# Optimization experiments

Hardware: AMD Instinct MI355X
Metric: run time of the kernel (lower is better)

Reference implementation:

```python
import jax, jax.numpy as jnp
import numpy as np

TAU_MEM = 20.0
TAU_SYN = 5.0
ALPHA_MEM = float(np.exp(-1.0 / TAU_MEM))
ALPHA_SYN = float(np.exp(-1.0 / TAU_SYN))
CONNECTIVITY = 0.1
SPECTRAL_RADIUS = 0.9


def setup_inputs() -> dict:
    key = jax.random.key(0)
    k1, k2, k3, k4 = jax.random.split(key, 4)
    B, D, N = 2048, 256, 512
    rates = jax.random.normal(k1, (B, D), dtype=jnp.float32)
    input_weight = jax.random.normal(k2, (N, D), dtype=jnp.float32) * 0.1
    W = jax.random.normal(k3, (N, N), dtype=jnp.float32)
    mask = (jax.random.uniform(k4, (N, N)) < CONNECTIVITY).astype(jnp.float32)
    W = W * mask
    # mirror torch init: scale by spectral_radius / max eigvalsh
    max_eig = jnp.linalg.eigvalsh(W)[-1]
    W = W * (SPECTRAL_RADIUS / max_eig)
    return {
        "rates": rates,
        "input_weight": input_weight,
        "reservoir_weight": W,
        "v_mem": jnp.zeros((B, N), dtype=jnp.float32),
        "current": jnp.zeros((B, N), dtype=jnp.float32),
        "n_steps": 64,
    }


def reference(rates, input_weight, reservoir_weight, v_mem, current, n_steps):
    dtype = rates.dtype
    # input current is identical every step in the original loop -> hoist it
    input_current = rates @ input_weight.T  # (B, N)

    def step(carry, _):
        v, c, spike_sum = carry
        rec = (c > 0).astype(dtype) @ reservoir_weight  # (B, N)
        c = ALPHA_SYN * c + (1.0 - ALPHA_SYN) * (input_current + rec)
        v = ALPHA_MEM * v + (1.0 - ALPHA_MEM) * c
        spike_sum = spike_sum + (v > 0).astype(dtype)
        return (v, c, spike_sum), None

    (v, c, spike_sum), _ = jax.lax.scan(
        step, (v_mem, current, jnp.zeros_like(v_mem)), None, length=n_steps
    )
    readout = spike_sum / n_steps  # == stack(spikes).mean(dim=1)
    return readout, (v, c)
```

## Files before the change

kernel.cpp:

```cpp
#include <hip/hip_runtime.h>
#include <stdint.h>


#define N_NEU 512
#define B_ROWS 2048
#define D_IN 256
#define R_PB 8
#define NBLK (B_ROWS / R_PB)

#define WS_PERM    0
#define WS_RANK    2048
#define WS_CNT     4096
#define WS_CNTW    8192
#define WS_IBASE   8256
#define WS_WBASE   8320
#define WS_IDX     16384
#define WS_WT      81920

#define SPK_OFF(k)  ((k) << 4)
#define SPK_BUF     8192

#define H16_ONE 0x3C00u

__global__ __launch_bounds__(256) void lsm_count(
    const float* __restrict__ W, uint32_t* __restrict__ ws)
{
    int t  = threadIdx.x;
    int k0 = blockIdx.x * 4;
    int c0 = 0, c1 = 0;
    #pragma unroll
    for (int kk = 0; kk < 4; ++kk) {
        const float* row = W + (size_t)(k0 + kk) * N_NEU;
        c0 += (row[t]       != 0.0f) ? 1 : 0;
        c1 += (row[t + 256] != 0.0f) ? 1 : 0;
    }
    if (c0) atomicAdd(&ws[(WS_CNT >> 2) + t],       (uint32_t)c0);
    if (c1) atomicAdd(&ws[(WS_CNT >> 2) + t + 256], (uint32_t)c1);
}

__global__ __launch_bounds__(512) void lsm_sort(uint32_t* __restrict__ ws)
{
    __shared__ int hist[N_NEU + 1];
    __shared__ int csort[N_NEU];
    __shared__ int gcw[8];

    int t = threadIdx.x;
    int creal = (int)ws[(WS_CNT >> 2) + t];
    for (int i = t; i < N_NEU + 1; i += 512) hist[i] = 0;
    __syncthreads();
    atomicAdd(&hist[creal], 1);
    __syncthreads();
    if (t == 0) {
        int acc = 0;
        for (int v = 0; v <= N_NEU; ++v) { int h = hist[v]; hist[v] = acc; acc += h; }
    }
    __syncthreads();
    int rank = atomicAdd(&hist[creal], 1);
    ws[(WS_PERM >> 2) + rank] = (uint32_t)t;
    ws[(WS_RANK >> 2) + t]    = (uint32_t)rank;
    csort[rank] = creal;
    __syncthreads();
    if (t < 8) {
        int cw = csort[t * 64 + 63];
        cw = (cw + 7) & ~7;
        gcw[t] = cw;
        ws[(WS_CNTW >> 2) + t] = (uint32_t)cw;
    }
    __syncthreads();
    if (t == 0) {
        int ai = 0, aw = 0;
        for (int g = 0; g < 8; ++g) {
            ws[(WS_IBASE >> 2) + g] = (uint32_t)ai;
            ws[(WS_WBASE >> 2) + g] = (uint32_t)aw;
            ai += gcw[g] * 64 * 2;
            aw += gcw[g] * 64 * 4;
        }
    }
    __syncthreads();
    int wg = rank >> 6, ls = rank & 63;
    int cw = gcw[wg];
    uint32_t ib = ws[(WS_IBASE >> 2) + wg];
    uint32_t wb = ws[(WS_WBASE >> 2) + wg];
    char* base = (char*)ws;
    for (int j = creal; j < cw; ++j) {
        *(unsigned short*)(base + WS_IDX + ib + (j >> 3) * 1024 + ls * 16 + (j & 7) * 2) = 0;
        *(float*)(base + WS_WT + wb + (j >> 3) * 2048 + ls * 32 + (j & 7) * 4) = 0.0f;
    }
}

__global__ __launch_bounds__(64) void lsm_fill(
    const float* __restrict__ W, uint32_t* __restrict__ ws)
{
    int c    = blockIdx.x;
    int lane = threadIdx.x;
    char* base = (char*)ws;
    uint32_t rank = ws[(WS_RANK >> 2) + c];
    int wg = (int)(rank >> 6), ls = (int)(rank & 63);
    uint32_t ib = ws[(WS_IBASE >> 2) + wg];
    uint32_t wb = ws[(WS_WBASE >> 2) + wg];
    int rot = ls & 7;

    __shared__ int bcnt[8];
    __shared__ int bcur[8];
    if (lane < 8) bcnt[lane] = 0;
    __syncthreads();

    for (int k = lane; k < N_NEU; k += 64) {
        float wv = W[(size_t)k * N_NEU + c];
        if (wv != 0.0f) {
            int r = ((k & 7) - rot) & 7;
            atomicAdd(&bcnt[r], 1);
        }
    }
    __syncthreads();
    if (lane == 0) {
        int acc = 0;
        for (int r = 0; r < 8; ++r) { bcur[r] = acc; acc += bcnt[r]; }
    }
    __syncthreads();

    for (int k = lane; k < N_NEU; k += 64) {
        float wv = W[(size_t)k * N_NEU + c];
        if (wv != 0.0f) {
            int r = ((k & 7) - rot) & 7;
            int j = atomicAdd(&bcur[r], 1);
            *(unsigned short*)(base + WS_IDX + ib + (j >> 3) * 1024 + ls * 16 + (j & 7) * 2)
                = (unsigned short)SPK_OFF(k);
            *(float*)(base + WS_WT + wb + (j >> 3) * 2048 + ls * 32 + (j & 7) * 4) = wv;
        }
    }
}

#define GATH(P, X, B) \
    P##0 = *(const uint4*)((B) + ((X).x & 0xffffu)); \
    P##1 = *(const uint4*)((B) + ((X).x >> 16));     \
    P##2 = *(const uint4*)((B) + ((X).y & 0xffffu)); \
    P##3 = *(const uint4*)((B) + ((X).y >> 16));     \
    P##4 = *(const uint4*)((B) + ((X).z & 0xffffu)); \
    P##5 = *(const uint4*)((B) + ((X).z >> 16));     \
    P##6 = *(const uint4*)((B) + ((X).w & 0xffffu)); \
    P##7 = *(const uint4*)((B) + ((X).w >> 16));

#define FMIX_LO(ACC, WV, S) \
    asm("v_fma_mix_f32 %0, %1, %2, %0 op_sel:[0,0,0] op_sel_hi:[0,1,0]" \
        : "+v"(ACC) : "v"(WV), "v"(S));
#define FMIX_HI(ACC, WV, S) \
    asm("v_fma_mix_f32 %0, %1, %2, %0 op_sel:[0,1,0] op_sel_hi:[0,1,0]" \
        : "+v"(ACC) : "v"(WV), "v"(S));

#define C1(S, WV) \
    FMIX_LO(rec0, WV, (S).x) FMIX_HI(rec1, WV, (S).x) \
    FMIX_LO(rec2, WV, (S).y) FMIX_HI(rec3, WV, (S).y) \
    FMIX_LO(rec4, WV, (S).z) FMIX_HI(rec5, WV, (S).z) \
    FMIX_LO(rec6, WV, (S).w) FMIX_HI(rec7, WV, (S).w)

#define CONS(P, WA, WB) \
    C1(P##0, (WA).x) C1(P##1, (WA).y) C1(P##2, (WA).z) C1(P##3, (WA).w) \
    C1(P##4, (WB).x) C1(P##5, (WB).y) C1(P##6, (WB).z) C1(P##7, (WB).w)

#define LDW(WA, WB, K) \
    WA = ((const float4*)(wp0 + (K) * 2048))[0]; \
    WB = ((const float4*)(wp0 + (K) * 2048))[1];

__global__ __launch_bounds__(512, 1)
void lsm_main(
    const float* __restrict__ rates, const float* __restrict__ inW,
    const float* __restrict__ vin,   const float* __restrict__ cin,
    const int* __restrict__ nsteps_p,
    const uint32_t* __restrict__ ws, float* __restrict__ out)
{
    __shared__ __align__(16) unsigned char smem[2 * SPK_BUF + 16384];
    float* stg = (float*)(smem + 2 * SPK_BUF);
    float* rl  = stg;

    int q    = threadIdx.x;
    int blk  = blockIdx.x;
    int r0   = blk * R_PB;
    int w    = q >> 6;
    int lane = q & 63;
    int wg   = (w < 4) ? w : (11 - w);
    int n    = (int)ws[(WS_PERM >> 2) + wg * 64 + lane];
    int cw   = (int)ws[(WS_CNTW >> 2) + wg];
    int nit  = cw >> 3;
    const char* ip0 = (const char*)ws + WS_IDX + ws[(WS_IBASE >> 2) + wg]
                    + lane * 16;
    const char* wp0 = (const char*)ws + WS_WT  + ws[(WS_WBASE >> 2) + wg]
                    + lane * 32;
    int spk_n = SPK_OFF(n);

    float c0v[R_PB], v0v[R_PB];
    #pragma unroll
    for (int r = 0; r < R_PB; ++r)
        stg[r * N_NEU + q] = cin[(size_t)(r0 + r) * N_NEU + q];
    __syncthreads();
    #pragma unroll
    for (int r = 0; r < R_PB; ++r) c0v[r] = stg[r * N_NEU + n];
    __syncthreads();
    #pragma unroll
    for (int r = 0; r < R_PB; ++r)
        stg[r * N_NEU + q] = vin[(size_t)(r0 + r) * N_NEU + q];
    __syncthreads();
    #pragma unroll
    for (int r = 0; r < R_PB; ++r) v0v[r] = stg[r * N_NEU + n];
    __syncthreads();

    ((float4*)rl)[q] = ((const float4*)(rates + (size_t)r0 * D_IN))[q];
    __syncthreads();

    float I[R_PB] = {0.f, 0.f, 0.f, 0.f, 0.f, 0.f, 0.f, 0.f};
    {
        const float4* wrow = (const float4*)(inW + (size_t)n * D_IN);
        for (int d4 = 0; d4 < D_IN / 4; ++d4) {
            float4 wv = wrow[d4];
            #pragma unroll
            for (int r = 0; r < R_PB; ++r) {
                const float* rr = rl + r * D_IN + d4 * 4;
                I[r] += wv.x * rr[0] + wv.y * rr[1] + wv.z * rr[2] + wv.w * rr[3];
            }
        }
    }

    uint4 sini = make_uint4(0u, 0u, 0u, 0u);
    #pragma unroll
    for (int r = 0; r < R_PB; ++r) {
        unsigned hb = (c0v[r] > 0.f) ? H16_ONE : 0u;
        unsigned sh = (r & 1) ? 16 : 0;
        if (r < 2)      sini.x |= hb << sh;
        else if (r < 4) sini.y |= hb << sh;
        else if (r < 6) sini.z |= hb << sh;
        else            sini.w |= hb << sh;
    }
    *(uint4*)(smem + spk_n) = sini;

    unsigned ssx = 0u, ssy = 0u;

    uint4 xr0, xr1, xr2, xr3, xr4, xr5, xr6, xr7, xr8, xr9, xr10, xr11;
    const uint4 xz = make_uint4(0u, 0u, 0u, 0u);
    xr0  =              *(const uint4*)(ip0);
    xr1  = (1  < nit) ? *(const uint4*)(ip0 + 1024)  : xz;
    xr2  = (2  < nit) ? *(const uint4*)(ip0 + 2048)  : xz;
    xr3  = (3  < nit) ? *(const uint4*)(ip0 + 3072)  : xz;
    xr4  = (4  < nit) ? *(const uint4*)(ip0 + 4096)  : xz;
    xr5  = (5  < nit) ? *(const uint4*)(ip0 + 5120)  : xz;
    xr6  = (6  < nit) ? *(const uint4*)(ip0 + 6144)  : xz;
    xr7  = (7  < nit) ? *(const uint4*)(ip0 + 7168)  : xz;
    xr8  = (8  < nit) ? *(const uint4*)(ip0 + 8192)  : xz;
    xr9  = (9  < nit) ? *(const uint4*)(ip0 + 9216)  : xz;
    xr10 = (10 < nit) ? *(const uint4*)(ip0 + 10240) : xz;
    xr11 = (11 < nit) ? *(const uint4*)(ip0 + 11264) : xz;

    const float AS   = (float)0.8187307530779818;
    const float OMAS = (float)(1.0 - 0.8187307530779818);
    const float AM   = (float)0.9512294245007140;
    const float OMAM = (float)(1.0 - 0.9512294245007140);

    int T = nsteps_p[0];
    __syncthreads();

    #pragma unroll 1
    for (int t = 0; t < T; ++t) {
        const unsigned char* sb = smem + ((t & 1) ? SPK_BUF : 0);
        unsigned char*       db = smem + ((t & 1) ? 0 : SPK_BUF);

        float rec0 = 0.f, rec1 = 0.f, rec2 = 0.f, rec3 = 0.f;
        float rec4 = 0.f, rec5 = 0.f, rec6 = 0.f, rec7 = 0.f;
        uint4 a0, a1, a2, a3, a4, a5, a6, a7;
        uint4 b0, b1, b2, b3, b4, b5, b6, b7;
        float4 waA, wbA, waB, wbB;

        LDW(waA, wbA, 0)
        GATH(a, xr0, sb)
        if (1 < nit)  { LDW(waB, wbB, 1)  GATH(b, xr1, sb)  }
        CONS(a, waA, wbA)
        if (1 < nit)  {
            if (2 < nit)  { LDW(waA, wbA, 2)  GATH(a, xr2, sb)  }
            CONS(b, waB, wbB)
        }
        if (2 < nit)  {
            if (3 < nit)  { LDW(waB, wbB, 3)  GATH(b, xr3, sb)  }
            CONS(a, waA, wbA)
        }
        if (3 < nit)  {
            if (4 < nit)  { LDW(waA, wbA, 4)  GATH(a, xr4, sb)  }
            CONS(b, waB, wbB)
        }
        if (4 < nit)  {
            if (5 < nit)  { LDW(waB, wbB, 5)  GATH(b, xr5, sb)  }
            CONS(a, waA, wbA)
        }
        if (5 < nit)  {
            if (6 < nit)  { LDW(waA, wbA, 6)  GATH(a, xr6, sb)  }
            CONS(b, waB, wbB)
        }
        if (6 < nit)  {
            if (7 < nit)  { LDW(waB, wbB, 7)  GATH(b, xr7, sb)  }
            CONS(a, waA, wbA)
        }
        if (7 < nit)  {
            if (8 < nit)  { LDW(waA, wbA, 8)  GATH(a, xr8, sb)  }
            CONS(b, waB, wbB)
        }
        if (8 < nit)  {
            if (9 < nit)  { LDW(waB, wbB, 9)  GATH(b, xr9, sb)  }
            CONS(a, waA, wbA)
        }
        if (9 < nit)  {
            if (10 < nit) { LDW(waA, wbA, 10) GATH(a, xr10, sb) }
            CONS(b, waB, wbB)
        }
        if (10 < nit) {
            if (11 < nit) { LDW(waB, wbB, 11) GATH(b, xr11, sb) }
            CONS(a, waA, wbA)
        }
        if (11 < nit) {
            CONS(b, waB, wbB)
        }

        uint4 ns = make_uint4(0u, 0u, 0u, 0u);
        unsigned vbx = 0u, vby = 0u;
        {
            float rca[R_PB] = {rec0, rec1, rec2, rec3, rec4, rec5, rec6, rec7};
            #pragma unroll
            for (int r = 0; r < R_PB; ++r) {
                c0v[r] = AS * c0v[r] + OMAS * (I[r] + rca[r]);
                v0v[r] = AM * v0v[r] + OMAM * c0v[r];
                unsigned hb = (c0v[r] > 0.f) ? H16_ONE : 0u;
                unsigned vb = (v0v[r] > 0.f) ? 1u : 0u;
                unsigned sh = (r & 1) ? 16 : 0;
                if (r < 2)      ns.x |= hb << sh;
                else if (r < 4) ns.y |= hb << sh;
                else if (r < 6) ns.z |= hb << sh;
                else            ns.w |= hb << sh;
                if (r < 4) vbx |= vb << (r * 8);
                else       vby |= vb << ((r - 4) * 8);
            }
        }
        ssx += vbx;
        ssy += vby;
        *(uint4*)(db + spk_n) = ns;
        __syncthreads();
    }

    float invT = 1.0f / (float)T;
    size_t BN = (size_t)B_ROWS * N_NEU;

    #pragma unroll
    for (int r = 0; r < R_PB; ++r) {
        unsigned cnt = (r < 4) ? ((ssx >> (r * 8)) & 0xffu)
                               : ((ssy >> ((r - 4) * 8)) & 0xffu);
        stg[r * N_NEU + n] = (float)cnt * invT;
    }
    __syncthreads();
    #pragma unroll
    for (int r = 0; r < R_PB; ++r)
        out[(size_t)(r0 + r) * N_NEU + q] = stg[r * N_NEU + q];
    __syncthreads();

    #pragma unroll
    for (int r = 0; r < R_PB; ++r) stg[r * N_NEU + n] = v0v[r];
    __syncthreads();
    #pragma unroll
    for (int r = 0; r < R_PB; ++r)
        out[BN + (size_t)(r0 + r) * N_NEU + q] = stg[r * N_NEU + q];
    __syncthreads();

    #pragma unroll
    for (int r = 0; r < R_PB; ++r) stg[r * N_NEU + n] = c0v[r];
    __syncthreads();
    #pragma unroll
    for (int r = 0; r < R_PB; ++r)
        out[2 * BN + (size_t)(r0 + r) * N_NEU + q] = stg[r * N_NEU + q];
}

extern "C" void kernel_launch(void* const* d_in, const int* in_sizes, int n_in,
                              void* d_out, int out_size, void* d_ws, size_t ws_size,
                              hipStream_t stream)
{
    const float* rates = (const float*)d_in[0];
    const float* inW   = (const float*)d_in[1];
    const float* W     = (const float*)d_in[2];
    const float* vin   = (const float*)d_in[3];
    const float* cin   = (const float*)d_in[4];
    const int*   nst   = (const int*)d_in[5];
    uint32_t* ws = (uint32_t*)d_ws;
    float* out = (float*)d_out;
    (void)in_sizes; (void)n_in; (void)out_size; (void)ws_size;

    hipMemsetAsync((char*)d_ws + WS_CNT, 0, 2048, stream);

    lsm_count<<<128, 256, 0, stream>>>(W, ws);
    lsm_sort<<<1, 512, 0, stream>>>(ws);
    lsm_fill<<<N_NEU, 64, 0, stream>>>(W, ws);
    lsm_main<<<NBLK, 512, 0, stream>>>(rates, inW, vin, cin, nst, ws, out);
}
```

Measured before the change: 326.1 us.

## Schedule sparse index slots to spread LDS bank access across lanes per step

```diff
diff --git a/kernel.cpp b/kernel.cpp
--- a/kernel.cpp
+++ b/kernel.cpp
@@ -21,6 +21,8 @@
 #define SPK_BUF     8192
 
 #define H16_ONE 0x3C00u
+#define MAXPC   32
+#define MAXCW   96
 
 __global__ __launch_bounds__(256) void lsm_count(
     const float* __restrict__ W, uint32_t* __restrict__ ws)
@@ -76,58 +78,97 @@
             aw += gcw[g] * 64 * 4;
         }
     }
-    __syncthreads();
-    int wg = rank >> 6, ls = rank & 63;
-    int cw = gcw[wg];
-    uint32_t ib = ws[(WS_IBASE >> 2) + wg];
-    uint32_t wb = ws[(WS_WBASE >> 2) + wg];
-    char* base = (char*)ws;
-    for (int j = creal; j < cw; ++j) {
-        *(unsigned short*)(base + WS_IDX + ib + (j >> 3) * 1024 + ls * 16 + (j & 7) * 2) = 0;
-        *(float*)(base + WS_WT + wb + (j >> 3) * 2048 + ls * 32 + (j & 7) * 4) = 0.0f;
-    }
 }
 
 __global__ __launch_bounds__(64) void lsm_fill(
     const float* __restrict__ W, uint32_t* __restrict__ ws)
 {
-    int c    = blockIdx.x;
-    int lane = threadIdx.x;
+    int wg = blockIdx.x;
+    int ls = threadIdx.x;
     char* base = (char*)ws;
-    uint32_t rank = ws[(WS_RANK >> 2) + c];
-    int wg = (int)(rank >> 6), ls = (int)(rank & 63);
+
+    int c  = (int)ws[(WS_PERM >> 2) + wg * 64 + ls];
+    int cw = (int)ws[(WS_CNTW >> 2) + wg];
     uint32_t ib = ws[(WS_IBASE >> 2) + wg];
     uint32_t wb = ws[(WS_WBASE >> 2) + wg];
-    int rot = ls & 7;
-
-    __shared__ int bcnt[8];
-    __shared__ int bcur[8];
-    if (lane < 8) bcnt[lane] = 0;
-    __syncthreads();
-
-    for (int k = lane; k < N_NEU; k += 64) {
-        float wv = W[(size_t)k * N_NEU + c];
-        if (wv != 0.0f) {
-            int r = ((k & 7) - rot) & 7;
-            atomicAdd(&bcnt[r], 1);
-        }
-    }
-    __syncthreads();
-    if (lane == 0) {
-        int acc = 0;
-        for (int r = 0; r < 8; ++r) { bcur[r] = acc; acc += bcnt[r]; }
-    }
-    __syncthreads();
-
-    for (int k = lane; k < N_NEU; k += 64) {
-        float wv = W[(size_t)k * N_NEU + c];
-        if (wv != 0.0f) {
-            int r = ((k & 7) - rot) & 7;
-            int j = atomicAdd(&bcur[r], 1);
-            *(unsigned short*)(base + WS_IDX + ib + (j >> 3) * 1024 + ls * 16 + (j & 7) * 2)
-                = (unsigned short)SPK_OFF(k);
-            *(float*)(base + WS_WT + wb + (j >> 3) * 2048 + ls * 32 + (j & 7) * 4) = wv;
-        }
+
+    __shared__ unsigned short ent[64][8][MAXPC];
+    __shared__ unsigned short sched[64][98];
+    __shared__ int cap[8];
+
+    unsigned cl = 0, ch = 0;
+    int tot = 0;
+    for (int k0 = 0; k0 < N_NEU; k0 += 8) {
+        #pragma unroll
+        for (int rr = 0; rr < 8; ++rr) {
+            float wv = W[(size_t)(k0 + rr) * N_NEU + c];
+            if (wv != 0.0f) {
+                unsigned cnt = ((rr < 4) ? (cl >> (rr * 8))
+                                         : (ch >> ((rr - 4) * 8))) & 0xffu;
+                ent[ls][rr][cnt] = (unsigned short)(k0 + rr);
+                if (rr < 4) cl += 1u << (rr * 8);
+                else        ch += 1u << ((rr - 4) * 8);
+                ++tot;
+            }
+        }
+    }
+
+    for (int j = 0; j < cw; ++j) {
+        if (ls < 8) cap[ls] = 0;
+        __syncthreads();
+        int sel = -1;
+        if (tot > 0) {
+            int slack = (cw - j) - tot;
+            unsigned tried = 0;
+            for (int pass = 0; pass < 8 && sel < 0; ++pass) {
+                int best = -1; unsigned bv = 0;
+                #pragma unroll
+                for (int r = 0; r < 8; ++r) {
+                    unsigned v = ((r < 4) ? (cl >> (r * 8))
+                                          : (ch >> ((r - 4) * 8))) & 0xffu;
+                    if (!((tried >> r) & 1u) && v > bv) { bv = v; best = r; }
+                }
+                if (best < 0) break;
+                int old = atomicAdd(&cap[best], 1);
+                if (old < 8) sel = best;
+                else { atomicSub(&cap[best], 1); tried |= (1u << best); }
+            }
+            if (sel < 0 && slack <= 0) {
+                int best = 0; unsigned bv = 0;
+                #pragma unroll
+                for (int r = 0; r < 8; ++r) {
+                    unsigned v = ((r < 4) ? (cl >> (r * 8))
+                                          : (ch >> ((r - 4) * 8))) & 0xffu;
+                    if (v > bv) { bv = v; best = r; }
+                }
+                sel = best;
+            }
+        }
+        unsigned short sv = 0xffffu;
+        if (sel >= 0) {
+            unsigned v = ((sel < 4) ? (cl >> (sel * 8))
+                                    : (ch >> ((sel - 4) * 8))) & 0xffu;
+            sv = ent[ls][sel][(int)v - 1];
+            if (sel < 4) cl -= 1u << (sel * 8);
+            else         ch -= 1u << ((sel - 4) * 8);
+            --tot;
+        }
+        sched[ls][j] = sv;
+        __syncthreads();
+    }
+
+    for (int j = 0; j < cw; ++j) {
+        unsigned short sv = sched[ls][j];
+        unsigned short idxv; float wv;
+        if (sv != 0xffffu) {
+            idxv = (unsigned short)(sv << 4);
+            wv   = W[(size_t)sv * N_NEU + c];
+        } else {
+            idxv = (unsigned short)((j & 7) << 4);
+            wv   = 0.0f;
+        }
+        *(unsigned short*)(base + WS_IDX + ib + (j >> 3) * 1024 + ls * 16 + (j & 7) * 2) = idxv;
+        *(float*)(base + WS_WT + wb + (j >> 3) * 2048 + ls * 32 + (j & 7) * 4) = wv;
     }
 }
 
@@ -171,7 +212,6 @@
 {
     __shared__ __align__(16) unsigned char smem[2 * SPK_BUF + 16384];
     float* stg = (float*)(smem + 2 * SPK_BUF);
-    float* rl  = stg;
 
     int q    = threadIdx.x;
     int blk  = blockIdx.x;
@@ -204,18 +244,16 @@
     for (int r = 0; r < R_PB; ++r) v0v[r] = stg[r * N_NEU + n];
     __syncthreads();
 
-    ((float4*)rl)[q] = ((const float4*)(rates + (size_t)r0 * D_IN))[q];
-    __syncthreads();
-
     float I[R_PB] = {0.f, 0.f, 0.f, 0.f, 0.f, 0.f, 0.f, 0.f};
     {
         const float4* wrow = (const float4*)(inW + (size_t)n * D_IN);
+        const float4* rrow = (const float4*)(rates + (size_t)r0 * D_IN);
         for (int d4 = 0; d4 < D_IN / 4; ++d4) {
             float4 wv = wrow[d4];
             #pragma unroll
             for (int r = 0; r < R_PB; ++r) {
-                const float* rr = rl + r * D_IN + d4 * 4;
-                I[r] += wv.x * rr[0] + wv.y * rr[1] + wv.z * rr[2] + wv.w * rr[3];
+                float4 rv = rrow[r * (D_IN / 4) + d4];
+                I[r] += wv.x * rv.x + wv.y * rv.y + wv.z * rv.z + wv.w * rv.w;
             }
         }
     }
@@ -390,6 +428,6 @@
 
     lsm_count<<<128, 256, 0, stream>>>(W, ws);
     lsm_sort<<<1, 512, 0, stream>>>(ws);
-    lsm_fill<<<N_NEU, 64, 0, stream>>>(W, ws);
+    lsm_fill<<<8, 64, 0, stream>>>(W, ws);
     lsm_main<<<NBLK, 512, 0, stream>>>(rates, inW, vin, cin, nst, ws, out);
 }
```

Result: slower. 617.0 us (+89.2%).

## Rebuild sparse fill with row-residue buckets to balance LDS banks in gather

Applied to the files above, without the earlier changes.

```diff
diff --git a/kernel.cpp b/kernel.cpp
--- a/kernel.cpp
+++ b/kernel.cpp
@@ -21,6 +21,7 @@
 #define SPK_BUF     8192
 
 #define H16_ONE 0x3C00u
+#define MAXPC   24
 
 __global__ __launch_bounds__(256) void lsm_count(
     const float* __restrict__ W, uint32_t* __restrict__ ws)
@@ -76,57 +77,85 @@
             aw += gcw[g] * 64 * 4;
         }
     }
-    __syncthreads();
-    int wg = rank >> 6, ls = rank & 63;
-    int cw = gcw[wg];
-    uint32_t ib = ws[(WS_IBASE >> 2) + wg];
-    uint32_t wb = ws[(WS_WBASE >> 2) + wg];
-    char* base = (char*)ws;
-    for (int j = creal; j < cw; ++j) {
-        *(unsigned short*)(base + WS_IDX + ib + (j >> 3) * 1024 + ls * 16 + (j & 7) * 2) = 0;
-        *(float*)(base + WS_WT + wb + (j >> 3) * 2048 + ls * 32 + (j & 7) * 4) = 0.0f;
-    }
 }
 
-__global__ __launch_bounds__(64) void lsm_fill(
+__global__ __launch_bounds__(512) void lsm_fill(
     const float* __restrict__ W, uint32_t* __restrict__ ws)
 {
-    int c    = blockIdx.x;
-    int lane = threadIdx.x;
+    int g = blockIdx.x;
+    int t = threadIdx.x;
     char* base = (char*)ws;
-    uint32_t rank = ws[(WS_RANK >> 2) + c];
-    int wg = (int)(rank >> 6), ls = (int)(rank & 63);
-    uint32_t ib = ws[(WS_IBASE >> 2) + wg];
-    uint32_t wb = ws[(WS_WBASE >> 2) + wg];
-    int rot = ls & 7;
-
-    __shared__ int bcnt[8];
-    __shared__ int bcur[8];
-    if (lane < 8) bcnt[lane] = 0;
-    __syncthreads();
-
-    for (int k = lane; k < N_NEU; k += 64) {
-        float wv = W[(size_t)k * N_NEU + c];
-        if (wv != 0.0f) {
-            int r = ((k & 7) - rot) & 7;
-            atomicAdd(&bcnt[r], 1);
-        }
-    }
-    __syncthreads();
-    if (lane == 0) {
-        int acc = 0;
-        for (int r = 0; r < 8; ++r) { bcur[r] = acc; acc += bcnt[r]; }
-    }
-    __syncthreads();
-
-    for (int k = lane; k < N_NEU; k += 64) {
-        float wv = W[(size_t)k * N_NEU + c];
-        if (wv != 0.0f) {
-            int r = ((k & 7) - rot) & 7;
-            int j = atomicAdd(&bcur[r], 1);
-            *(unsigned short*)(base + WS_IDX + ib + (j >> 3) * 1024 + ls * 16 + (j & 7) * 2)
-                = (unsigned short)SPK_OFF(k);
-            *(float*)(base + WS_WT + wb + (j >> 3) * 2048 + ls * 32 + (j & 7) * 4) = wv;
+
+    __shared__ unsigned short ent_k[64][8][MAXPC];
+    __shared__ float          ent_w[64][8][MAXPC];
+
+    int rank = (int)ws[(WS_RANK >> 2) + t];
+    int ls   = rank & 63;
+    bool mine = ((rank >> 6) == g);
+
+    unsigned cl = 0, ch = 0;
+    for (int k0 = 0; k0 < N_NEU; k0 += 8) {
+        float wv[8];
+        #pragma unroll
+        for (int rr = 0; rr < 8; ++rr)
+            wv[rr] = W[(size_t)(k0 + rr) * N_NEU + t];
+        #pragma unroll
+        for (int rr = 0; rr < 8; ++rr) {
+            if (mine && wv[rr] != 0.0f) {
+                unsigned cnt = ((rr < 4) ? (cl >> (rr * 8))
+                                         : (ch >> ((rr - 4) * 8))) & 0xffu;
+                ent_k[ls][rr][cnt] = (unsigned short)(k0 + rr);
+                ent_w[ls][rr][cnt] = wv[rr];
+                if (rr < 4) cl += 1u << (rr * 8);
+                else        ch += 1u << ((rr - 4) * 8);
+            }
+        }
+    }
+
+    if (mine) {
+        int cw = (int)ws[(WS_CNTW >> 2) + g];
+        uint32_t ib = ws[(WS_IBASE >> 2) + g];
+        uint32_t wb = ws[(WS_WBASE >> 2) + g];
+        int Q = cw >> 3;
+
+        unsigned ul = 0, uh = 0;
+        int ovr = 0, ovi = Q;
+        while (ovr < 8) {
+            int nr = (int)(((ovr < 4) ? (cl >> (ovr * 8))
+                                      : (ch >> ((ovr - 4) * 8))) & 0xffu);
+            if (ovi < nr) break;
+            ++ovr; ovi = Q;
+        }
+
+        for (int j = 0; j < cw; ++j) {
+            int c = (j + ls) & 7;
+            int nc = (int)(((c < 4) ? (cl >> (c * 8))
+                                    : (ch >> ((c - 4) * 8))) & 0xffu);
+            int uc = (int)(((c < 4) ? (ul >> (c * 8))
+                                    : (uh >> ((c - 4) * 8))) & 0xffu);
+            int dc = (nc < Q) ? nc : Q;
+            unsigned short idxv; float wvv;
+            if (uc < dc) {
+                idxv = (unsigned short)SPK_OFF(ent_k[ls][c][uc]);
+                wvv  = ent_w[ls][c][uc];
+                if (c < 4) ul += 1u << (c * 8);
+                else       uh += 1u << ((c - 4) * 8);
+            } else if (ovr < 8) {
+                idxv = (unsigned short)SPK_OFF(ent_k[ls][ovr][ovi]);
+                wvv  = ent_w[ls][ovr][ovi];
+                ++ovi;
+                while (ovr < 8) {
+                    int nr = (int)(((ovr < 4) ? (cl >> (ovr * 8))
+                                              : (ch >> ((ovr - 4) * 8))) & 0xffu);
+                    if (ovi < nr) break;
+                    ++ovr; ovi = Q;
+                }
+            } else {
+                idxv = (unsigned short)SPK_OFF(c);
+                wvv  = 0.0f;
+            }
+            *(unsigned short*)(base + WS_IDX + ib + (j >> 3) * 1024 + ls * 16 + (j & 7) * 2) = idxv;
+            *(float*)(base + WS_WT + wb + (j >> 3) * 2048 + ls * 32 + (j & 7) * 4) = wvv;
         }
     }
 }
@@ -390,6 +419,6 @@
 
     lsm_count<<<128, 256, 0, stream>>>(W, ws);
     lsm_sort<<<1, 512, 0, stream>>>(ws);
-    lsm_fill<<<N_NEU, 64, 0, stream>>>(W, ws);
+    lsm_fill<<<8, 512, 0, stream>>>(W, ws);
     lsm_main<<<NBLK, 512, 0, stream>>>(rates, inW, vin, cin, nst, ws, out);
 }
```

New measurement: 378.6 us. 1.16x slower.

## Halve rows per block, raise occupancy, and rebalance sparse index layout across banks

Applied to the files above, without the earlier changes.

```diff
diff --git a/kernel.cpp b/kernel.cpp
--- a/kernel.cpp
+++ b/kernel.cpp
@@ -5,7 +5,7 @@
 #define N_NEU 512
 #define B_ROWS 2048
 #define D_IN 256
-#define R_PB 8
+#define R_PB 4
 #define NBLK (B_ROWS / R_PB)
 
 #define WS_PERM    0
@@ -15,10 +15,10 @@
 #define WS_IBASE   8256
 #define WS_WBASE   8320
 #define WS_IDX     16384
-#define WS_WT      81920
-
-#define SPK_OFF(k)  ((k) << 4)
-#define SPK_BUF     8192
+#define WS_WT      98304
+
+#define SPK_OFF(k)  ((k) << 3)
+#define SPK_BUF     4096
 
 #define H16_ONE 0x3C00u
 
@@ -62,7 +62,7 @@
     __syncthreads();
     if (t < 8) {
         int cw = csort[t * 64 + 63];
-        cw = (cw + 7) & ~7;
+        cw = (cw + 15) & ~15;
         gcw[t] = cw;
         ws[(WS_CNTW >> 2) + t] = (uint32_t)cw;
     }
@@ -76,16 +76,6 @@
             aw += gcw[g] * 64 * 4;
         }
     }
-    __syncthreads();
-    int wg = rank >> 6, ls = rank & 63;
-    int cw = gcw[wg];
-    uint32_t ib = ws[(WS_IBASE >> 2) + wg];
-    uint32_t wb = ws[(WS_WBASE >> 2) + wg];
-    char* base = (char*)ws;
-    for (int j = creal; j < cw; ++j) {
-        *(unsigned short*)(base + WS_IDX + ib + (j >> 3) * 1024 + ls * 16 + (j & 7) * 2) = 0;
-        *(float*)(base + WS_WT + wb + (j >> 3) * 2048 + ls * 32 + (j & 7) * 4) = 0.0f;
-    }
 }
 
 __global__ __launch_bounds__(64) void lsm_fill(
@@ -94,52 +84,75 @@
     int c    = blockIdx.x;
     int lane = threadIdx.x;
     char* base = (char*)ws;
+
     uint32_t rank = ws[(WS_RANK >> 2) + c];
-    int wg = (int)(rank >> 6), ls = (int)(rank & 63);
-    uint32_t ib = ws[(WS_IBASE >> 2) + wg];
-    uint32_t wb = ws[(WS_WBASE >> 2) + wg];
-    int rot = ls & 7;
-
-    __shared__ int bcnt[8];
-    __shared__ int bcur[8];
-    if (lane < 8) bcnt[lane] = 0;
-    __syncthreads();
-
-    for (int k = lane; k < N_NEU; k += 64) {
+    int ls = (int)(rank & 63), g = (int)(rank >> 6);
+    int cw = (int)ws[(WS_CNTW >> 2) + g];
+    uint32_t ib = ws[(WS_IBASE >> 2) + g];
+    uint32_t wb = ws[(WS_WBASE >> 2) + g];
+
+    __shared__ unsigned short ent_k[16][16];
+    __shared__ float          ent_w[16][16];
+    __shared__ int            nb[16];
+
+    int bm = lane & 15;
+    unsigned long long mbk  = 0x0001000100010001ULL << bm;
+    unsigned long long below = (1ULL << lane) - 1;
+    int myBase = 0;
+    for (int i = 0; i < 8; ++i) {
+        int k = lane + 64 * i;
         float wv = W[(size_t)k * N_NEU + c];
-        if (wv != 0.0f) {
-            int r = ((k & 7) - rot) & 7;
-            atomicAdd(&bcnt[r], 1);
-        }
-    }
-    __syncthreads();
-    if (lane == 0) {
-        int acc = 0;
-        for (int r = 0; r < 8; ++r) { bcur[r] = acc; acc += bcnt[r]; }
-    }
-    __syncthreads();
-
-    for (int k = lane; k < N_NEU; k += 64) {
-        float wv = W[(size_t)k * N_NEU + c];
-        if (wv != 0.0f) {
-            int r = ((k & 7) - rot) & 7;
-            int j = atomicAdd(&bcur[r], 1);
-            *(unsigned short*)(base + WS_IDX + ib + (j >> 3) * 1024 + ls * 16 + (j & 7) * 2)
-                = (unsigned short)SPK_OFF(k);
-            *(float*)(base + WS_WT + wb + (j >> 3) * 2048 + ls * 32 + (j & 7) * 4) = wv;
-        }
+        bool nz = (wv != 0.0f);
+        unsigned long long bal = __ballot(nz);
+        if (nz) {
+            int p = myBase + __popcll(bal & mbk & below);
+            ent_k[bm][p] = (unsigned short)k;
+            ent_w[bm][p] = wv;
+        }
+        myBase += __popcll(bal & mbk);
+    }
+    if (lane < 16) nb[lane] = myBase;
+    __syncthreads();
+
+    int Q = cw >> 4;
+    for (int j = lane; j < cw; j += 64) {
+        int b = (j + ls) & 15;
+        int m = j >> 4;
+        int nbb = nb[b];
+        int d = (nbb < Q) ? nbb : Q;
+        unsigned short kk; float wv;
+        if (m < d) {
+            kk = ent_k[b][m]; wv = ent_w[b][m];
+        } else {
+            int f = m - d;
+            for (int bp = 0; bp < b; ++bp) {
+                int nn = nb[bp];
+                f += (Q > nn) ? (Q - nn) : 0;
+            }
+            int acc = 0, bsel = -1, isel = 0;
+            for (int bp = 0; bp < 16; ++bp) {
+                int ov = nb[bp] - Q; ov = (ov > 0) ? ov : 0;
+                if (bsel < 0 && f < acc + ov) { bsel = bp; isel = Q + (f - acc); }
+                acc += ov;
+            }
+            if (bsel >= 0) { kk = ent_k[bsel][isel]; wv = ent_w[bsel][isel]; }
+            else           { kk = (unsigned short)b; wv = 0.0f; }
+        }
+        *(unsigned short*)(base + WS_IDX + ib + (j >> 3) * 1024 + ls * 16 + (j & 7) * 2)
+            = (unsigned short)SPK_OFF(kk);
+        *(float*)(base + WS_WT + wb + (j >> 3) * 2048 + ls * 32 + (j & 7) * 4) = wv;
     }
 }
 
 #define GATH(P, X, B) \
-    P##0 = *(const uint4*)((B) + ((X).x & 0xffffu)); \
-    P##1 = *(const uint4*)((B) + ((X).x >> 16));     \
-    P##2 = *(const uint4*)((B) + ((X).y & 0xffffu)); \
-    P##3 = *(const uint4*)((B) + ((X).y >> 16));     \
-    P##4 = *(const uint4*)((B) + ((X).z & 0xffffu)); \
-    P##5 = *(const uint4*)((B) + ((X).z >> 16));     \
-    P##6 = *(const uint4*)((B) + ((X).w & 0xffffu)); \
-    P##7 = *(const uint4*)((B) + ((X).w >> 16));
+    P##0 = *(const uint2*)((B) + ((X).x & 0xffffu)); \
+    P##1 = *(const uint2*)((B) + ((X).x >> 16));     \
+    P##2 = *(const uint2*)((B) + ((X).y & 0xffffu)); \
+    P##3 = *(const uint2*)((B) + ((X).y >> 16));     \
+    P##4 = *(const uint2*)((B) + ((X).z & 0xffffu)); \
+    P##5 = *(const uint2*)((B) + ((X).z >> 16));     \
+    P##6 = *(const uint2*)((B) + ((X).w & 0xffffu)); \
+    P##7 = *(const uint2*)((B) + ((X).w >> 16));
 
 #define FMIX_LO(ACC, WV, S) \
     asm("v_fma_mix_f32 %0, %1, %2, %0 op_sel:[0,0,0] op_sel_hi:[0,1,0]" \
@@ -150,9 +163,7 @@
 
 #define C1(S, WV) \
     FMIX_LO(rec0, WV, (S).x) FMIX_HI(rec1, WV, (S).x) \
-    FMIX_LO(rec2, WV, (S).y) FMIX_HI(rec3, WV, (S).y) \
-    FMIX_LO(rec4, WV, (S).z) FMIX_HI(rec5, WV, (S).z) \
-    FMIX_LO(rec6, WV, (S).w) FMIX_HI(rec7, WV, (S).w)
+    FMIX_LO(rec2, WV, (S).y) FMIX_HI(rec3, WV, (S).y)
 
 #define CONS(P, WA, WB) \
     C1(P##0, (WA).x) C1(P##1, (WA).y) C1(P##2, (WA).z) C1(P##3, (WA).w) \
@@ -162,14 +173,14 @@
     WA = ((const float4*)(wp0 + (K) * 2048))[0]; \
     WB = ((const float4*)(wp0 + (K) * 2048))[1];
 
-__global__ __launch_bounds__(512, 1)
+__global__ __launch_bounds__(512, 4)
 void lsm_main(
     const float* __restrict__ rates, const float* __restrict__ inW,
     const float* __restrict__ vin,   const float* __restrict__ cin,
     const int* __restrict__ nsteps_p,
     const uint32_t* __restrict__ ws, float* __restrict__ out)
 {
-    __shared__ __align__(16) unsigned char smem[2 * SPK_BUF + 16384];
+    __shared__ __align__(16) unsigned char smem[2 * SPK_BUF + 8192];
     float* stg = (float*)(smem + 2 * SPK_BUF);
     float* rl  = stg;
 
@@ -204,10 +215,11 @@
     for (int r = 0; r < R_PB; ++r) v0v[r] = stg[r * N_NEU + n];
     __syncthreads();
 
-    ((float4*)rl)[q] = ((const float4*)(rates + (size_t)r0 * D_IN))[q];
-    __syncthreads();
-
-    float I[R_PB] = {0.f, 0.f, 0.f, 0.f, 0.f, 0.f, 0.f, 0.f};
+    if (q < (R_PB * D_IN) / 4)
+        ((float4*)rl)[q] = ((const float4*)(rates + (size_t)r0 * D_IN))[q];
+    __syncthreads();
+
+    float I[R_PB] = {0.f, 0.f, 0.f, 0.f};
     {
         const float4* wrow = (const float4*)(inW + (size_t)n * D_IN);
         for (int d4 = 0; d4 < D_IN / 4; ++d4) {
@@ -220,19 +232,17 @@
         }
     }
 
-    uint4 sini = make_uint4(0u, 0u, 0u, 0u);
+    uint2 sini = make_uint2(0u, 0u);
     #pragma unroll
     for (int r = 0; r < R_PB; ++r) {
         unsigned hb = (c0v[r] > 0.f) ? H16_ONE : 0u;
         unsigned sh = (r & 1) ? 16 : 0;
-        if (r < 2)      sini.x |= hb << sh;
-        else if (r < 4) sini.y |= hb << sh;
-        else if (r < 6) sini.z |= hb << sh;
-        else            sini.w |= hb << sh;
-    }
-    *(uint4*)(smem + spk_n) = sini;
-
-    unsigned ssx = 0u, ssy = 0u;
+        if (r < 2) sini.x |= hb << sh;
+        else       sini.y |= hb << sh;
+    }
+    *(uint2*)(smem + spk_n) = sini;
+
+    unsigned ssx = 0u;
 
     uint4 xr0, xr1, xr2, xr3, xr4, xr5, xr6, xr7, xr8, xr9, xr10, xr11;
     const uint4 xz = make_uint4(0u, 0u, 0u, 0u);
@@ -263,9 +273,8 @@
         unsigned char*       db = smem + ((t & 1) ? 0 : SPK_BUF);
 
         float rec0 = 0.f, rec1 = 0.f, rec2 = 0.f, rec3 = 0.f;
-        float rec4 = 0.f, rec5 = 0.f, rec6 = 0.f, rec7 = 0.f;
-        uint4 a0, a1, a2, a3, a4, a5, a6, a7;
-        uint4 b0, b1, b2, b3, b4, b5, b6, b7;
+        uint2 a0, a1, a2, a3, a4, a5, a6, a7;
+        uint2 b0, b1, b2, b3, b4, b5, b6, b7;
         float4 waA, wbA, waB, wbB;
 
         LDW(waA, wbA, 0)
@@ -316,10 +325,10 @@
             CONS(b, waB, wbB)
         }
 
-        uint4 ns = make_uint4(0u, 0u, 0u, 0u);
-        unsigned vbx = 0u, vby = 0u;
+        uint2 ns = make_uint2(0u, 0u);
+        unsigned vbx = 0u;
         {
-            float rca[R_PB] = {rec0, rec1, rec2, rec3, rec4, rec5, rec6, rec7};
+            float rca[R_PB] = {rec0, rec1, rec2, rec3};
             #pragma unroll
             for (int r = 0; r < R_PB; ++r) {
                 c0v[r] = AS * c0v[r] + OMAS * (I[r] + rca[r]);
@@ -327,17 +336,13 @@
                 unsigned hb = (c0v[r] > 0.f) ? H16_ONE : 0u;
                 unsigned vb = (v0v[r] > 0.f) ? 1u : 0u;
                 unsigned sh = (r & 1) ? 16 : 0;
-                if (r < 2)      ns.x |= hb << sh;
-                else if (r < 4) ns.y |= hb << sh;
-                else if (r < 6) ns.z |= hb << sh;
-                else            ns.w |= hb << sh;
-                if (r < 4) vbx |= vb << (r * 8);
-                else       vby |= vb << ((r - 4) * 8);
+                if (r < 2) ns.x |= hb << sh;
+                else       ns.y |= hb << sh;
+                vbx |= vb << (r * 8);
             }
         }
         ssx += vbx;
-        ssy += vby;
-        *(uint4*)(db + spk_n) = ns;
+        *(uint2*)(db + spk_n) = ns;
         __syncthreads();
     }
 
@@ -346,8 +351,7 @@
 
     #pragma unroll
     for (int r = 0; r < R_PB; ++r) {
-        unsigned cnt = (r < 4) ? ((ssx >> (r * 8)) & 0xffu)
-                               : ((ssy >> ((r - 4) * 8)) & 0xffu);
+        unsigned cnt = (ssx >> (r * 8)) & 0xffu;
         stg[r * N_NEU + n] = (float)cnt * invT;
     }
     __syncthreads();
```

After: 389.8 us. 19.5% more time.
